# Performance work log

Hardware: AMD Instinct MI355X
Metric: run time of the kernel (lower is better)

## Reference

```python
import jax, jax.numpy as jnp
import numpy as np

B, C, H, W = 2, 3, 96, 96
D = 32  # qkv channels

def setup_inputs() -> dict:
    key = jax.random.key(0)
    ks = jax.random.split(key, 9)
    s3 = 1.0 / np.sqrt(3.0)
    sD = 1.0 / np.sqrt(float(D))
    return {
        "image": jax.random.normal(ks[0], (B, C, H, W), dtype=jnp.float32),
        "key_w": jax.random.normal(ks[1], (D, C), dtype=jnp.float32) * s3,
        "key_b": jax.random.normal(ks[2], (D,), dtype=jnp.float32) * 0.01,
        "query_w": jax.random.normal(ks[3], (D, C), dtype=jnp.float32) * s3,
        "query_b": jax.random.normal(ks[4], (D,), dtype=jnp.float32) * 0.01,
        "value_w": jax.random.normal(ks[5], (D, C), dtype=jnp.float32) * s3,
        "value_b": jax.random.normal(ks[6], (D,), dtype=jnp.float32) * 0.01,
        "out_w": jax.random.normal(ks[7], (C, D), dtype=jnp.float32) * sD,
        "out_b": jax.random.normal(ks[8], (C,), dtype=jnp.float32) * 0.01,
    }

def reference(image, key_w, key_b, query_w, query_b, value_w, value_b, out_w, out_b):
    b, c, h, w = image.shape
    n = h * w
    x = image.reshape(b, c, n)  # [B,3,N]
    # 1x1 convs == per-pixel linear maps over channels
    f_x = jnp.einsum('dc,bcn->bdn', key_w, x) + key_b[None, :, None]    # key   [B,D,N]
    g_x = jnp.einsum('dc,bcn->bdn', query_w, x) + query_b[None, :, None]  # query [B,D,N]
    h_x = jnp.einsum('dc,bcn->bdn', value_w, x) + value_b[None, :, None]  # value [B,D,N]
    # s = f_x^T @ g_x : [B,N,N]; softmax over dim=1 (first N axis), as in torch code
    s = jnp.einsum('bdn,bdm->bnm', f_x, g_x)
    beta = jax.nn.softmax(s, axis=1)
    # v = h_x @ beta : [B,D,N]
    v = jnp.einsum('bdn,bnm->bdm', h_x, beta)
    # output 1x1 conv D->3, then clamp
    o = jnp.einsum('cd,bdm->bcm', out_w, v) + out_b[None, :, None]
    o = jnp.clip(o, -1.0, 1.0)
    return o.reshape(b, c, h, w)
```

## Files before the change

### kernel.cpp

```cpp
#include <hip/hip_runtime.h>
#include <hip/hip_fp16.h>

#define BB 2
#define CC 3
#define NN 9216
#define DD 32
#define NSPLIT 8
#define KSPLIT 2
#define KEYS_PER_WAVE (NN / (KSPLIT * NSPLIT))
#define CHUNKS (KEYS_PER_WAVE / 64)
#define NGROUP (BB * NN / 32)
#define L2E 1.44269504f

typedef _Float16 half8 __attribute__((ext_vector_type(8)));
typedef _Float16 half4v __attribute__((ext_vector_type(4)));
typedef __fp16 fp16x2 __attribute__((ext_vector_type(2)));
typedef float float4v __attribute__((ext_vector_type(4)));

#define MFMA_K32(a, b, c) __builtin_amdgcn_mfma_f32_16x16x32_f16((a), (b), (c), 0, 0, 0)

__global__ __launch_bounds__(256) void prep_kernel(
    const float* __restrict__ img,
    const float* __restrict__ kw, const float* __restrict__ kb,
    const float* __restrict__ qw, const float* __restrict__ qb,
    const float* __restrict__ vw, const float* __restrict__ vb,
    const float* __restrict__ ow,
    _Float16* __restrict__ fH, _Float16* __restrict__ fL,
    _Float16* __restrict__ gH, _Float16* __restrict__ gL,
    _Float16* __restrict__ hP)
{
    __shared__ float cwb[12];
    int bid = blockIdx.x;
    if (bid < 288) {
        int id = bid * 256 + threadIdx.x;
        int part = id & 3;
        int n = (id >> 2) % NN;
        int b = (id >> 2) / NN;
        const float* xb = img + (size_t)b * CC * NN + n;
        float x0 = xb[0], x1 = xb[NN], x2 = xb[2 * NN];
        half8 fh, fl, gh, gl;
#pragma unroll
        for (int j = 0; j < 8; j++) {
            int d = part * 8 + j;
            float fv = kw[d * 3 + 0] * x0 + kw[d * 3 + 1] * x1 + kw[d * 3 + 2] * x2 + kb[d];
            float gv = (qw[d * 3 + 0] * x0 + qw[d * 3 + 1] * x1 + qw[d * 3 + 2] * x2 + qb[d]) * L2E;
            _Float16 fhi = (_Float16)fv;
            _Float16 ghi = (_Float16)gv;
            fh[j] = fhi; fl[j] = (_Float16)(fv - (float)fhi);
            gh[j] = ghi; gl[j] = (_Float16)(gv - (float)ghi);
        }
        size_t off = ((size_t)b * NN + n) * DD + part * 8;
        *(half8*)(fH + off) = fh;
        *(half8*)(fL + off) = fl;
        *(half8*)(gH + off) = gh;
        *(half8*)(gL + off) = gl;
    } else {
        int t = threadIdx.x;
        if (t < 9) {
            int c = t / 3, k = t % 3;
            float s = 0.f;
#pragma unroll
            for (int d = 0; d < DD; d++) s += ow[c * DD + d] * vw[d * 3 + k];
            cwb[t] = s;
        } else if (t < 12) {
            int c = t - 9;
            float s = 0.f;
#pragma unroll
            for (int d = 0; d < DD; d++) s += ow[c * DD + d] * vb[d];
            cwb[9 + c] = s;
        }
        __syncthreads();
        const int N8 = NN / 8;
        int id = (bid - 288) * 256 + t;
        int n8 = id % N8;
        int row = (id / N8) & 3;
        int b = id / (N8 * 4);
        half8 hv = {0, 0, 0, 0, 0, 0, 0, 0};
        if (row < 3) {
            const float* xb = img + (size_t)b * CC * NN + n8 * 8;
            float w0 = cwb[row * 3 + 0], w1 = cwb[row * 3 + 1],
                  w2 = cwb[row * 3 + 2], bv = cwb[9 + row];
#pragma unroll
            for (int j = 0; j < 8; j++)
                hv[j] = (_Float16)(w0 * xb[j] + w1 * xb[NN + j] + w2 * xb[2 * NN + j] + bv);
        }
        *(half8*)(hP + ((size_t)(b * 4 + row)) * NN + n8 * 8) = hv;
    }
}

__global__ __launch_bounds__(512, 4) void attn_partial_kernel(
    const _Float16* __restrict__ fH, const _Float16* __restrict__ fL,
    const _Float16* __restrict__ gH, const _Float16* __restrict__ gL,
    const _Float16* __restrict__ hP,
    float* __restrict__ pnum, float* __restrict__ pM, float* __restrict__ pL)
{
    const int gb = blockIdx.x;
    const int g  = gb >> 1;
    const int ks = gb & 1;
    const int b = g / (NN / 32);
    const int m0 = (g % (NN / 32)) * 32;
    const int tid = threadIdx.x;
    const int w = tid >> 6;
    const int lane = tid & 63;
    const int l16 = lane & 15;
    const int quad = lane >> 4;

    union SMem {
        _Float16 P[NSPLIT * 2 * 16 * 72];
        float acc[NSPLIT][CC][33];
    };
    __shared__ __align__(16) SMem sm;
    __shared__ float mbuf[NSPLIT][32];
    __shared__ float lbuf[NSPLIT][4][32];

    const _Float16* gHb = gH + ((size_t)b * NN + m0 + l16) * DD + quad * 8;
    const _Float16* gLb = gL + ((size_t)b * NN + m0 + l16) * DD + quad * 8;
    half8 qh0 = *(const half8*)(gHb);
    half8 ql0 = *(const half8*)(gLb);
    half8 qh1 = *(const half8*)(gHb + (size_t)16 * DD);
    half8 ql1 = *(const half8*)(gLb + (size_t)16 * DD);

    float4v acc0 = {0,0,0,0};
    float4v acc1 = {0,0,0,0};
    float mrun0 = -1e30f, lrun0 = 0.f;
    float mrun1 = -1e30f, lrun1 = 0.f;

    const int nbase = ks * (NN / KSPLIT) + w * KEYS_PER_WAVE;
    const int vrow = (l16 < 3) ? l16 : 3;
    const _Float16* vp = hP + ((size_t)(b * 4 + vrow)) * NN + nbase + quad * 8;
    const _Float16* khp = fH + ((size_t)b * NN + nbase + l16) * DD + quad * 8;
    const _Float16* klp = fL + ((size_t)b * NN + nbase + l16) * DD + quad * 8;
    _Float16* Pw0 = sm.P + (size_t)(w * 2 + 0) * 16 * 72;
    _Float16* Pw1 = sm.P + (size_t)(w * 2 + 1) * 16 * 72;

    for (int c = 0; c < CHUNKS; ++c) {
        half8 ka[4], kl[4];
#pragma unroll
        for (int blk = 0; blk < 4; blk++) {
            ka[blk] = *(const half8*)(khp + (size_t)(c * 64 + blk * 16) * DD);
            kl[blk] = *(const half8*)(klp + (size_t)(c * 64 + blk * 16) * DD);
        }
        half8 vA0 = *(const half8*)(vp + c * 64);
        half8 vA1 = *(const half8*)(vp + c * 64 + 32);

        {
            float4v s[4];
#pragma unroll
            for (int blk = 0; blk < 4; blk++) {
                float4v z = {0,0,0,0};
                float4v t = MFMA_K32(ka[blk], ql0, z);
                t = MFMA_K32(kl[blk], qh0, t);
                s[blk] = MFMA_K32(ka[blk], qh0, t);
            }
            float mb0 = fmaxf(fmaxf(s[0][0], s[0][1]), fmaxf(s[0][2], s[0][3]));
            float mb1 = fmaxf(fmaxf(s[1][0], s[1][1]), fmaxf(s[1][2], s[1][3]));
            float mb2 = fmaxf(fmaxf(s[2][0], s[2][1]), fmaxf(s[2][2], s[2][3]));
            float mb3 = fmaxf(fmaxf(s[3][0], s[3][1]), fmaxf(s[3][2], s[3][3]));
            float mx = fmaxf(fmaxf(mb0, mb1), fmaxf(mb2, mb3));
            mx = fmaxf(mx, __shfl_xor(mx, 16, 64));
            mx = fmaxf(mx, __shfl_xor(mx, 32, 64));
            float mnew = fmaxf(mrun0, mx);
            float rsum = 0.f;
#pragma unroll
            for (int blk = 0; blk < 4; blk++) {
                float p0 = __builtin_amdgcn_exp2f(s[blk][0] - mnew);
                float p1 = __builtin_amdgcn_exp2f(s[blk][1] - mnew);
                float p2 = __builtin_amdgcn_exp2f(s[blk][2] - mnew);
                float p3 = __builtin_amdgcn_exp2f(s[blk][3] - mnew);
                union { fp16x2 h2[2]; half4v h4; } u;
                u.h2[0] = __builtin_amdgcn_cvt_pkrtz(p0, p1);
                u.h2[1] = __builtin_amdgcn_cvt_pkrtz(p2, p3);
                *(half4v*)(Pw0 + l16 * 72 + blk * 16 + quad * 4) = u.h4;
                rsum += (p0 + p1) + (p2 + p3);
            }
            if (__any(mnew > mrun0)) {
                float alpha = __builtin_amdgcn_exp2f(mrun0 - mnew);
#pragma unroll
                for (int r = 0; r < 4; r++) acc0[r] *= alpha;
                lrun0 = lrun0 * alpha + rsum;
                mrun0 = mnew;
            } else {
                lrun0 += rsum;
            }
        }
        {
            float4v s[4];
#pragma unroll
            for (int blk = 0; blk < 4; blk++) {
                float4v z = {0,0,0,0};
                float4v t = MFMA_K32(ka[blk], ql1, z);
                t = MFMA_K32(kl[blk], qh1, t);
                s[blk] = MFMA_K32(ka[blk], qh1, t);
            }
            float mb0 = fmaxf(fmaxf(s[0][0], s[0][1]), fmaxf(s[0][2], s[0][3]));
            float mb1 = fmaxf(fmaxf(s[1][0], s[1][1]), fmaxf(s[1][2], s[1][3]));
            float mb2 = fmaxf(fmaxf(s[2][0], s[2][1]), fmaxf(s[2][2], s[2][3]));
            float mb3 = fmaxf(fmaxf(s[3][0], s[3][1]), fmaxf(s[3][2], s[3][3]));
            float mx = fmaxf(fmaxf(mb0, mb1), fmaxf(mb2, mb3));
            mx = fmaxf(mx, __shfl_xor(mx, 16, 64));
            mx = fmaxf(mx, __shfl_xor(mx, 32, 64));
            float mnew = fmaxf(mrun1, mx);
            float rsum = 0.f;
#pragma unroll
            for (int blk = 0; blk < 4; blk++) {
                float p0 = __builtin_amdgcn_exp2f(s[blk][0] - mnew);
                float p1 = __builtin_amdgcn_exp2f(s[blk][1] - mnew);
                float p2 = __builtin_amdgcn_exp2f(s[blk][2] - mnew);
                float p3 = __builtin_amdgcn_exp2f(s[blk][3] - mnew);
                union { fp16x2 h2[2]; half4v h4; } u;
                u.h2[0] = __builtin_amdgcn_cvt_pkrtz(p0, p1);
                u.h2[1] = __builtin_amdgcn_cvt_pkrtz(p2, p3);
                *(half4v*)(Pw1 + l16 * 72 + blk * 16 + quad * 4) = u.h4;
                rsum += (p0 + p1) + (p2 + p3);
            }
            if (__any(mnew > mrun1)) {
                float alpha = __builtin_amdgcn_exp2f(mrun1 - mnew);
#pragma unroll
                for (int r = 0; r < 4; r++) acc1[r] *= alpha;
                lrun1 = lrun1 * alpha + rsum;
                mrun1 = mnew;
            } else {
                lrun1 += rsum;
            }
        }
        {
            half8 pf0 = *(const half8*)(Pw0 + l16 * 72 + quad * 8);
            half8 pf1 = *(const half8*)(Pw0 + l16 * 72 + 32 + quad * 8);
            acc0 = MFMA_K32(vA0, pf0, acc0);
            acc0 = MFMA_K32(vA1, pf1, acc0);
            half8 qf0 = *(const half8*)(Pw1 + l16 * 72 + quad * 8);
            half8 qf1 = *(const half8*)(Pw1 + l16 * 72 + 32 + quad * 8);
            acc1 = MFMA_K32(vA0, qf0, acc1);
            acc1 = MFMA_K32(vA1, qf1, acc1);
        }
    }

    __syncthreads();

    mbuf[w][l16]            = mrun0;
    mbuf[w][l16 + 16]       = mrun1;
    lbuf[w][quad][l16]      = lrun0;
    lbuf[w][quad][l16 + 16] = lrun1;
    if (quad == 0) {
#pragma unroll
        for (int r = 0; r < 3; r++) {
            sm.acc[w][r][l16]      = acc0[r];
            sm.acc[w][r][l16 + 16] = acc1[r];
        }
    }
    __syncthreads();

    if (tid < CC * 32) {
        int c = tid >> 5, m = tid & 31;
        float M = mbuf[0][m];
#pragma unroll
        for (int s2 = 1; s2 < NSPLIT; s2++) M = fmaxf(M, mbuf[s2][m]);
        float L = 0.f, num = 0.f;
#pragma unroll
        for (int s2 = 0; s2 < NSPLIT; s2++) {
            float e2 = __builtin_amdgcn_exp2f(mbuf[s2][m] - M);
            float lsum = (lbuf[s2][0][m] + lbuf[s2][1][m]) + (lbuf[s2][2][m] + lbuf[s2][3][m]);
            L += lsum * e2;
            num += sm.acc[s2][c][m] * e2;
        }
        pnum[(size_t)gb * (CC * 32) + tid] = num;
        if (c == 0) { pM[gb * 32 + m] = M; pL[gb * 32 + m] = L; }
    }
}

__global__ __launch_bounds__(128) void merge_kernel(
    const float* __restrict__ pnum, const float* __restrict__ pM,
    const float* __restrict__ pL, const float* __restrict__ ob,
    float* __restrict__ out)
{
    const int g = blockIdx.x;
    const int b = g / (NN / 32);
    const int m0 = (g % (NN / 32)) * 32;
    const int tid = threadIdx.x;
    const int gb0 = g * 2, gb1 = g * 2 + 1;

    if (tid < CC * 32) {
        int c = tid >> 5, m = tid & 31;
        float M0 = pM[gb0 * 32 + m], M1 = pM[gb1 * 32 + m];
        float M = fmaxf(M0, M1);
        float e0 = __builtin_amdgcn_exp2f(M0 - M);
        float e1 = __builtin_amdgcn_exp2f(M1 - M);
        float L = pL[gb0 * 32 + m] * e0 + pL[gb1 * 32 + m] * e1;
        float num = pnum[(size_t)gb0 * (CC * 32) + tid] * e0 +
                    pnum[(size_t)gb1 * (CC * 32) + tid] * e1;
        float o = num / L + ob[c];
        o = fminf(1.f, fmaxf(-1.f, o));
        out[((size_t)b * CC + c) * NN + m0 + m] = o;
    }
}

extern "C" void kernel_launch(void* const* d_in, const int* in_sizes, int n_in,
                              void* d_out, int out_size, void* d_ws, size_t ws_size,
                              hipStream_t stream) {
    const float* img = (const float*)d_in[0];
    const float* kw  = (const float*)d_in[1];
    const float* kb  = (const float*)d_in[2];
    const float* qw  = (const float*)d_in[3];
    const float* qb  = (const float*)d_in[4];
    const float* vw  = (const float*)d_in[5];
    const float* vb  = (const float*)d_in[6];
    const float* ow  = (const float*)d_in[7];
    const float* ob  = (const float*)d_in[8];
    float* out = (float*)d_out;

    const size_t sz = (size_t)BB * NN * DD;
    _Float16* fH = (_Float16*)d_ws;
    _Float16* fL = fH + sz;
    _Float16* gH = fL + sz;
    _Float16* gL = gH + sz;
    _Float16* hP = gL + sz;
    float* pnum = (float*)(hP + (size_t)BB * 4 * NN);
    float* pM   = pnum + (size_t)NGROUP * KSPLIT * CC * 32;
    float* pL   = pM + (size_t)NGROUP * KSPLIT * 32;

    prep_kernel<<<324, 256, 0, stream>>>(img, kw, kb, qw, qb, vw, vb, ow,
                                         fH, fL, gH, gL, hP);
    attn_partial_kernel<<<NGROUP * KSPLIT, 512, 0, stream>>>(
        fH, fL, gH, gL, hP, pnum, pM, pL);
    merge_kernel<<<NGROUP, 128, 0, stream>>>(pnum, pM, pL, ob, out);
}
```

Measured before the change: 135.5 us.

## Fold softmax denominator into MFMA via ones row and rebalance key split

The padded fourth row of the value operand is now filled with ones, so the P·V MFMA also accumulates the softmax row sum in its fourth output row. This removes the per-chunk scalar rsum additions and the separate l-buffer bookkeeping. The work split changes from 8 waves × 2 key splits to 4 waves × 4 key splits with 256-thread blocks, and the merge kernel now combines four partials and reads L from the partial numerator buffer. The denominator is now summed from fp16-rounded P values, which slightly changes numerics, and the merge kernel does more global reads per output.

Result: slower. 322.4 us (+138.0%).

```diff
diff --git a/kernel.cpp b/kernel.cpp
--- a/kernel.cpp
+++ b/kernel.cpp
@@ -5,8 +5,8 @@
 #define CC 3
 #define NN 9216
 #define DD 32
-#define NSPLIT 8
-#define KSPLIT 2
+#define NSPLIT 4
+#define KSPLIT 4
 #define KEYS_PER_WAVE (NN / (KSPLIT * NSPLIT))
 #define CHUNKS (KEYS_PER_WAVE / 64)
 #define NGROUP (BB * NN / 32)
@@ -75,7 +75,7 @@
         int n8 = id % N8;
         int row = (id / N8) & 3;
         int b = id / (N8 * 4);
-        half8 hv = {0, 0, 0, 0, 0, 0, 0, 0};
+        half8 hv = {1, 1, 1, 1, 1, 1, 1, 1};
         if (row < 3) {
             const float* xb = img + (size_t)b * CC * NN + n8 * 8;
             float w0 = cwb[row * 3 + 0], w1 = cwb[row * 3 + 1],
@@ -88,15 +88,15 @@
     }
 }
 
-__global__ __launch_bounds__(512, 4) void attn_partial_kernel(
+__global__ __launch_bounds__(256, 8) void attn_partial_kernel(
     const _Float16* __restrict__ fH, const _Float16* __restrict__ fL,
     const _Float16* __restrict__ gH, const _Float16* __restrict__ gL,
     const _Float16* __restrict__ hP,
-    float* __restrict__ pnum, float* __restrict__ pM, float* __restrict__ pL)
+    float* __restrict__ pnum, float* __restrict__ pM)
 {
     const int gb = blockIdx.x;
-    const int g  = gb >> 1;
-    const int ks = gb & 1;
+    const int g  = gb >> 2;
+    const int ks = gb & 3;
     const int b = g / (NN / 32);
     const int m0 = (g % (NN / 32)) * 32;
     const int tid = threadIdx.x;
@@ -107,11 +107,9 @@
 
     union SMem {
         _Float16 P[NSPLIT * 2 * 16 * 72];
-        float acc[NSPLIT][CC][33];
+        struct { float acc[NSPLIT][4][33]; float mbuf[NSPLIT][32]; } mg;
     };
     __shared__ __align__(16) SMem sm;
-    __shared__ float mbuf[NSPLIT][32];
-    __shared__ float lbuf[NSPLIT][4][32];
 
     const _Float16* gHb = gH + ((size_t)b * NN + m0 + l16) * DD + quad * 8;
     const _Float16* gLb = gL + ((size_t)b * NN + m0 + l16) * DD + quad * 8;
@@ -122,8 +120,8 @@
 
     float4v acc0 = {0,0,0,0};
     float4v acc1 = {0,0,0,0};
-    float mrun0 = -1e30f, lrun0 = 0.f;
-    float mrun1 = -1e30f, lrun1 = 0.f;
+    float mrun0 = -1e30f;
+    float mrun1 = -1e30f;
 
     const int nbase = ks * (NN / KSPLIT) + w * KEYS_PER_WAVE;
     const int vrow = (l16 < 3) ? l16 : 3;
@@ -152,15 +150,17 @@
                 t = MFMA_K32(kl[blk], qh0, t);
                 s[blk] = MFMA_K32(ka[blk], qh0, t);
             }
-            float mb0 = fmaxf(fmaxf(s[0][0], s[0][1]), fmaxf(s[0][2], s[0][3]));
-            float mb1 = fmaxf(fmaxf(s[1][0], s[1][1]), fmaxf(s[1][2], s[1][3]));
-            float mb2 = fmaxf(fmaxf(s[2][0], s[2][1]), fmaxf(s[2][2], s[2][3]));
-            float mb3 = fmaxf(fmaxf(s[3][0], s[3][1]), fmaxf(s[3][2], s[3][3]));
-            float mx = fmaxf(fmaxf(mb0, mb1), fmaxf(mb2, mb3));
+            float mx = fmaxf(fmaxf(s[0][0], s[0][1]), s[0][2]);
+            mx = fmaxf(fmaxf(mx, s[0][3]), s[1][0]);
+            mx = fmaxf(fmaxf(mx, s[1][1]), s[1][2]);
+            mx = fmaxf(fmaxf(mx, s[1][3]), s[2][0]);
+            mx = fmaxf(fmaxf(mx, s[2][1]), s[2][2]);
+            mx = fmaxf(fmaxf(mx, s[2][3]), s[3][0]);
+            mx = fmaxf(fmaxf(mx, s[3][1]), s[3][2]);
+            mx = fmaxf(mx, s[3][3]);
             mx = fmaxf(mx, __shfl_xor(mx, 16, 64));
             mx = fmaxf(mx, __shfl_xor(mx, 32, 64));
             float mnew = fmaxf(mrun0, mx);
-            float rsum = 0.f;
 #pragma unroll
             for (int blk = 0; blk < 4; blk++) {
                 float p0 = __builtin_amdgcn_exp2f(s[blk][0] - mnew);
@@ -171,16 +171,12 @@
                 u.h2[0] = __builtin_amdgcn_cvt_pkrtz(p0, p1);
                 u.h2[1] = __builtin_amdgcn_cvt_pkrtz(p2, p3);
                 *(half4v*)(Pw0 + l16 * 72 + blk * 16 + quad * 4) = u.h4;
-                rsum += (p0 + p1) + (p2 + p3);
             }
             if (__any(mnew > mrun0)) {
                 float alpha = __builtin_amdgcn_exp2f(mrun0 - mnew);
 #pragma unroll
                 for (int r = 0; r < 4; r++) acc0[r] *= alpha;
-                lrun0 = lrun0 * alpha + rsum;
                 mrun0 = mnew;
-            } else {
-                lrun0 += rsum;
             }
         }
         {
@@ -192,15 +188,17 @@
                 t = MFMA_K32(kl[blk], qh1, t);
                 s[blk] = MFMA_K32(ka[blk], qh1, t);
             }
-            float mb0 = fmaxf(fmaxf(s[0][0], s[0][1]), fmaxf(s[0][2], s[0][3]));
-            float mb1 = fmaxf(fmaxf(s[1][0], s[1][1]), fmaxf(s[1][2], s[1][3]));
-            float mb2 = fmaxf(fmaxf(s[2][0], s[2][1]), fmaxf(s[2][2], s[2][3]));
-            float mb3 = fmaxf(fmaxf(s[3][0], s[3][1]), fmaxf(s[3][2], s[3][3]));
-            float mx = fmaxf(fmaxf(mb0, mb1), fmaxf(mb2, mb3));
+            float mx = fmaxf(fmaxf(s[0][0], s[0][1]), s[0][2]);
+            mx = fmaxf(fmaxf(mx, s[0][3]), s[1][0]);
+            mx = fmaxf(fmaxf(mx, s[1][1]), s[1][2]);
+            mx = fmaxf(fmaxf(mx, s[1][3]), s[2][0]);
+            mx = fmaxf(fmaxf(mx, s[2][1]), s[2][2]);
+            mx = fmaxf(fmaxf(mx, s[2][3]), s[3][0]);
+            mx = fmaxf(fmaxf(mx, s[3][1]), s[3][2]);
+            mx = fmaxf(mx, s[3][3]);
             mx = fmaxf(mx, __shfl_xor(mx, 16, 64));
             mx = fmaxf(mx, __shfl_xor(mx, 32, 64));
             float mnew = fmaxf(mrun1, mx);
-            float rsum = 0.f;
 #pragma unroll
             for (int blk = 0; blk < 4; blk++) {
                 float p0 = __builtin_amdgcn_exp2f(s[blk][0] - mnew);
@@ -211,16 +209,12 @@
                 u.h2[0] = __builtin_amdgcn_cvt_pkrtz(p0, p1);
                 u.h2[1] = __builtin_amdgcn_cvt_pkrtz(p2, p3);
                 *(half4v*)(Pw1 + l16 * 72 + blk * 16 + quad * 4) = u.h4;
-                rsum += (p0 + p1) + (p2 + p3);
             }
             if (__any(mnew > mrun1)) {
                 float alpha = __builtin_amdgcn_exp2f(mrun1 - mnew);
 #pragma unroll
                 for (int r = 0; r < 4; r++) acc1[r] *= alpha;
-                lrun1 = lrun1 * alpha + rsum;
                 mrun1 = mnew;
-            } else {
-                lrun1 += rsum;
             }
         }
         {
@@ -237,57 +231,53 @@
 
     __syncthreads();
 
-    mbuf[w][l16]            = mrun0;
-    mbuf[w][l16 + 16]       = mrun1;
-    lbuf[w][quad][l16]      = lrun0;
-    lbuf[w][quad][l16 + 16] = lrun1;
     if (quad == 0) {
 #pragma unroll
-        for (int r = 0; r < 3; r++) {
-            sm.acc[w][r][l16]      = acc0[r];
-            sm.acc[w][r][l16 + 16] = acc1[r];
-        }
+        for (int r = 0; r < 4; r++) {
+            sm.mg.acc[w][r][l16]      = acc0[r];
+            sm.mg.acc[w][r][l16 + 16] = acc1[r];
+        }
+        sm.mg.mbuf[w][l16]      = mrun0;
+        sm.mg.mbuf[w][l16 + 16] = mrun1;
     }
     __syncthreads();
 
-    if (tid < CC * 32) {
+    if (tid < 4 * 32) {
         int c = tid >> 5, m = tid & 31;
-        float M = mbuf[0][m];
-#pragma unroll
-        for (int s2 = 1; s2 < NSPLIT; s2++) M = fmaxf(M, mbuf[s2][m]);
-        float L = 0.f, num = 0.f;
-#pragma unroll
-        for (int s2 = 0; s2 < NSPLIT; s2++) {
-            float e2 = __builtin_amdgcn_exp2f(mbuf[s2][m] - M);
-            float lsum = (lbuf[s2][0][m] + lbuf[s2][1][m]) + (lbuf[s2][2][m] + lbuf[s2][3][m]);
-            L += lsum * e2;
-            num += sm.acc[s2][c][m] * e2;
-        }
-        pnum[(size_t)gb * (CC * 32) + tid] = num;
-        if (c == 0) { pM[gb * 32 + m] = M; pL[gb * 32 + m] = L; }
+        float M = sm.mg.mbuf[0][m];
+#pragma unroll
+        for (int s2 = 1; s2 < NSPLIT; s2++) M = fmaxf(M, sm.mg.mbuf[s2][m]);
+        float v = 0.f;
+#pragma unroll
+        for (int s2 = 0; s2 < NSPLIT; s2++)
+            v += sm.mg.acc[s2][c][m] * __builtin_amdgcn_exp2f(sm.mg.mbuf[s2][m] - M);
+        pnum[(size_t)gb * 128 + tid] = v;
+        if (c == 0) pM[gb * 32 + m] = M;
     }
 }
 
 __global__ __launch_bounds__(128) void merge_kernel(
     const float* __restrict__ pnum, const float* __restrict__ pM,
-    const float* __restrict__ pL, const float* __restrict__ ob,
-    float* __restrict__ out)
+    const float* __restrict__ ob, float* __restrict__ out)
 {
     const int g = blockIdx.x;
     const int b = g / (NN / 32);
     const int m0 = (g % (NN / 32)) * 32;
     const int tid = threadIdx.x;
-    const int gb0 = g * 2, gb1 = g * 2 + 1;
 
     if (tid < CC * 32) {
         int c = tid >> 5, m = tid & 31;
-        float M0 = pM[gb0 * 32 + m], M1 = pM[gb1 * 32 + m];
-        float M = fmaxf(M0, M1);
-        float e0 = __builtin_amdgcn_exp2f(M0 - M);
-        float e1 = __builtin_amdgcn_exp2f(M1 - M);
-        float L = pL[gb0 * 32 + m] * e0 + pL[gb1 * 32 + m] * e1;
-        float num = pnum[(size_t)gb0 * (CC * 32) + tid] * e0 +
-                    pnum[(size_t)gb1 * (CC * 32) + tid] * e1;
+        int base = g * KSPLIT;
+        float M = pM[base * 32 + m];
+#pragma unroll
+        for (int k = 1; k < KSPLIT; k++) M = fmaxf(M, pM[(base + k) * 32 + m]);
+        float num = 0.f, L = 0.f;
+#pragma unroll
+        for (int k = 0; k < KSPLIT; k++) {
+            float e = __builtin_amdgcn_exp2f(pM[(base + k) * 32 + m] - M);
+            num += pnum[(size_t)(base + k) * 128 + c * 32 + m] * e;
+            L   += pnum[(size_t)(base + k) * 128 + 96 + m] * e;
+        }
         float o = num / L + ob[c];
         o = fminf(1.f, fmaxf(-1.f, o));
         out[((size_t)b * CC + c) * NN + m0 + m] = o;
@@ -315,12 +305,11 @@
     _Float16* gL = gH + sz;
     _Float16* hP = gL + sz;
     float* pnum = (float*)(hP + (size_t)BB * 4 * NN);
-    float* pM   = pnum + (size_t)NGROUP * KSPLIT * CC * 32;
-    float* pL   = pM + (size_t)NGROUP * KSPLIT * 32;
+    float* pM   = pnum + (size_t)NGROUP * KSPLIT * 128;
 
     prep_kernel<<<324, 256, 0, stream>>>(img, kw, kb, qw, qb, vw, vb, ow,
                                          fH, fL, gH, gL, hP);
-    attn_partial_kernel<<<NGROUP * KSPLIT, 512, 0, stream>>>(
-        fH, fL, gH, gL, hP, pnum, pM, pL);
-    merge_kernel<<<NGROUP, 128, 0, stream>>>(pnum, pM, pL, ob, out);
+    attn_partial_kernel<<<NGROUP * KSPLIT, 256, 0, stream>>>(
+        fH, fL, gH, gL, hP, pnum, pM);
+    merge_kernel<<<NGROUP, 128, 0, stream>>>(pnum, pM, ob, out);
 }
```
